# Performance work log

Measured on AMD Instinct MI355X. Metric: run time of the kernel, lower is better.

The kernel has to match this reference:

```python
import jax, jax.numpy as jnp
import numpy as np

CP = 1.0   # polynomial kernel balance (Kerv2d cp)
DP = 2     # polynomial kernel degree (Kerv2d dp)
EPS = 1e-5 # BatchNorm eps


def kerv2d(x, w, stride, padding):
    # polynomial kervolution: (patch . w + cp) ** dp, computed as conv then pointwise
    y = jax.lax.conv_general_dilated(
        x, w,
        window_strides=(stride, stride),
        padding=[(padding, padding), (padding, padding)],
        dimension_numbers=('NCHW', 'OIHW', 'NCHW'))
    return (y + CP) ** DP


def bn(x, g, b, m, v):
    # inference-mode BatchNorm2d with running stats, folded to scale/shift
    inv = g / jnp.sqrt(v + EPS)
    return x * inv[None, :, None, None] + (b - m * inv)[None, :, None, None]


def setup_inputs() -> dict:
    key = jax.random.key(0)
    ks = jax.random.split(key, 4)
    C_in, C_mid = 1024, 256  # bottleneck: 1024 -> 256 -> 256 -> 1024
    d = {
        'x':  jax.random.normal(ks[0], (128, C_in, 14, 14), jnp.float32),
        'w1': jax.random.normal(ks[1], (C_mid, C_in, 1, 1), jnp.float32) * 0.03,
        'w2': jax.random.normal(ks[2], (C_mid, C_mid, 3, 3), jnp.float32) * 0.02,
        'w3': jax.random.normal(ks[3], (C_in, C_mid, 1, 1), jnp.float32) * 0.03,
    }
    for i, c in zip((1, 2, 3), (C_mid, C_mid, C_in)):
        d[f'g{i}'] = jnp.ones((c,), jnp.float32)
        d[f'b{i}'] = jnp.zeros((c,), jnp.float32)
        d[f'm{i}'] = jnp.zeros((c,), jnp.float32)
        d[f'v{i}'] = jnp.ones((c,), jnp.float32)
    return d


def reference(x, w1, w2, w3, g1, b1, m1, v1, g2, b2, m2, v2, g3, b3, m3, v3):
    identity = x
    h = bn(kerv2d(x, w1, 1, 0), g1, b1, m1, v1)   # 1x1 kerv + BN (num_layers>34 branch)
    h = bn(kerv2d(h, w2, 1, 1), g2, b2, m2, v2)   # 3x3 kerv + BN, stride=1
    h = bn(kerv2d(h, w3, 1, 0), g3, b3, m3, v3)   # 1x1 kerv (expansion=4) + BN
    return h + identity                           # residual add (identity_downsample=None)
```

## Files before the change

### kernel.cpp

```cpp
#include <hip/hip_runtime.h>

using f32x4 = __attribute__((ext_vector_type(4))) float;
using s16x8 = __attribute__((ext_vector_type(8))) short;
using s16x4 = __attribute__((ext_vector_type(4))) short;

#define P_PIX 196
#define NPIX_ALL (128 * 196)
#define NROW  208
#define KT    32

static __device__ __forceinline__ short f2bf(float f) {
  union { float f; unsigned u; } a; a.f = f;
  unsigned u = a.u;
  u += 0x7fffu + ((u >> 16) & 1u);
  return (short)(u >> 16);
}

static __device__ __forceinline__ f32x4 mfma16(s16x8 a, s16x8 b, f32x4 c) {
  return __builtin_amdgcn_mfma_f32_16x16x32_bf16(a, b, c, 0, 0, 0);
}

static __device__ __forceinline__ void gload16(const short* g, short* l) {
  __builtin_amdgcn_global_load_lds(
      (const __attribute__((address_space(1))) unsigned int*)(g),
      (__attribute__((address_space(3))) unsigned int*)(l), 16, 0, 0);
}

static __device__ __forceinline__ const s16x8* fragp(const short* buf, int row, int l4) {
  return (const s16x8*)(buf + row * KT + ((l4 ^ ((row >> 1) & 3)) << 3));
}

static __device__ __forceinline__ void stage(const short* __restrict__ src, int srcK,
                                             int k0, short* dst, int rows, int rmax,
                                             int tid, int nthr) {
  for (int t = tid; t < rows * 4; t += nthr) {
    int r = t >> 2, c = t & 3;
    int rr = r < rmax ? r : rmax;
    int cs = c ^ ((r >> 1) & 3);
    gload16(src + (size_t)rr * srcK + k0 + cs * 8, dst + t * 8);
  }
}


__global__ void k_prep(const float* __restrict__ w1, const float* __restrict__ w2,
                       const float* __restrict__ w3,
                       const float* g1, const float* b1, const float* m1, const float* v1,
                       const float* g2, const float* b2, const float* m2, const float* v2,
                       const float* g3, const float* b3, const float* m3, const float* v3,
                       float* bn, short* W1b, short* W2t, short* W3b) {
  int i = blockIdx.x * 256 + threadIdx.x;
  if (i < 65536) {
    f32x4 v = *(const f32x4*)(w1 + i * 4);
    s16x4 o;
    o[0] = f2bf(v[0]); o[1] = f2bf(v[1]); o[2] = f2bf(v[2]); o[3] = f2bf(v[3]);
    *(s16x4*)(W1b + i * 4) = o;
  } else if (i < 131072) {
    int q = i - 65536;
    f32x4 v = *(const f32x4*)(w3 + q * 4);
    s16x4 o;
    o[0] = f2bf(v[0]); o[1] = f2bf(v[1]); o[2] = f2bf(v[2]); o[3] = f2bf(v[3]);
    *(s16x4*)(W3b + q * 4) = o;
  } else if (i < 278528) {
    int q = (i - 131072) * 4;
    s16x4 o;
    #pragma unroll
    for (int k = 0; k < 4; ++k) {
      int idx = q + k;
      int s = idx >> 16, rem = idx & 65535;
      int co = rem >> 8, ci = rem & 255;
      o[k] = f2bf(w2[(co * 256 + ci) * 9 + s]);
    }
    *(s16x4*)(W2t + q) = o;
  } else if (i < 280064) {
    int t = i - 278528;
    if (t < 256) {
      float inv = g1[t] * rsqrtf(v1[t] + 1e-5f);
      bn[t] = inv; bn[256 + t] = b1[t] - m1[t] * inv;
    } else if (t < 512) {
      int c = t - 256;
      float inv = g2[c] * rsqrtf(v2[c] + 1e-5f);
      bn[512 + c] = inv; bn[768 + c] = b2[c] - m2[c] * inv;
    } else {
      int c = t - 512;
      float inv = g3[c] * rsqrtf(v3[c] + 1e-5f);
      bn[1024 + c] = inv; bn[2048 + c] = b3[c] - m3[c] * inv;
    }
  }
}


__global__ __launch_bounds__(256) void k_layer1(
    const float* __restrict__ x, const short* __restrict__ W1b,
    const float* __restrict__ bnbuf, short* __restrict__ H1) {
  __shared__ __align__(16) short lB[2][128 * KT];
  const int tid = threadIdx.x;
  const int vb = (blockIdx.x & 7) * 64 + (blockIdx.x >> 3);
  const int n = vb >> 2, mb = (vb >> 1) & 1, jh = vb & 1;
  const int lane = tid & 63, wave = tid >> 6;
  const int l15 = lane & 15, l4 = lane >> 4;

  if (jh == 1 && tid < 96) {
    int bb = tid / 48, idx = tid % 48;
    s16x8 z = {0,0,0,0,0,0,0,0};
    *(s16x8*)(&lB[bb][100 * KT + idx * 8]) = z;
  }

  const float* xs = x + (size_t)n * 1024 * P_PIX;
  const short* Asrc = W1b + (size_t)(mb * 128) * 1024;

  const int npg = jh ? 25 : 28;
  const int pgbase = jh ? 24 : 0;
  const bool act = tid < npg * 8;
  const int pg = pgbase + (act ? tid % npg : 0);
  const int kg = act ? tid / npg : 0;
  const int lrow0 = pg * 4 - jh * 96;

  f32x4 rX[4], rY[4];
  auto loadx = [&](int kt, f32x4* r) {
    if (!act) return;
    const float* sp = xs + (size_t)(kt * 32 + kg * 4) * P_PIX + pg * 4;
    r[0] = *(const f32x4*)sp;
    r[1] = *(const f32x4*)(sp + P_PIX);
    r[2] = *(const f32x4*)(sp + 2 * P_PIX);
    r[3] = *(const f32x4*)(sp + 3 * P_PIX);
  };
  auto cvtw = [&](const f32x4* r, short* buf) {
    if (!act) return;
    int chunk = kg >> 1, inner = (kg & 1) * 4;
    #pragma unroll
    for (int q = 0; q < 4; ++q) {
      int lr = lrow0 + q;
      s16x4 w;
      w[0] = f2bf(r[0][q]); w[1] = f2bf(r[1][q]);
      w[2] = f2bf(r[2][q]); w[3] = f2bf(r[3][q]);
      *(s16x4*)(buf + lr * KT + ((chunk ^ ((lr >> 1) & 3)) << 3) + inner) = w;
    }
  };

  f32x4 acc[2][7];
  f32x4 zero = {0.f, 0.f, 0.f, 0.f};
  #pragma unroll
  for (int m = 0; m < 2; ++m)
    #pragma unroll
    for (int jj = 0; jj < 7; ++jj) acc[m][jj] = zero;

  loadx(0, rX);
  loadx(1, rY);
  cvtw(rX, lB[0]);
  __syncthreads();

  auto body = [&](int kt, f32x4* rNext, f32x4* rFill) {
    if (kt + 2 < 32) loadx(kt + 2, rFill);
    s16x8 a0 = *(const s16x8*)(Asrc + (size_t)(wave * 32 + l15) * 1024 + kt * 32 + l4 * 8);
    s16x8 a1 = *(const s16x8*)(Asrc + (size_t)(wave * 32 + 16 + l15) * 1024 + kt * 32 + l4 * 8);
    const short* B = lB[kt & 1];
    #pragma unroll
    for (int jj = 0; jj < 7; ++jj) {
      s16x8 bfr = *fragp(B, jj * 16 + l15, l4);
      acc[0][jj] = mfma16(a0, bfr, acc[0][jj]);
      acc[1][jj] = mfma16(a1, bfr, acc[1][jj]);
    }
    if (kt + 1 < 32) cvtw(rNext, lB[(kt + 1) & 1]);
    __syncthreads();
  };

  for (int kt = 0; kt < 32; kt += 2) {
    body(kt, rY, rX);
    body(kt + 1, rX, rY);
  }

  short* Hn = H1 + (size_t)n * P_PIX * 256;
  #pragma unroll
  for (int m = 0; m < 2; ++m) {
    int co = mb * 128 + wave * 32 + m * 16 + l4 * 4;
    f32x4 sc = *(const f32x4*)(bnbuf + co);
    f32x4 sh = *(const f32x4*)(bnbuf + 256 + co);
    #pragma unroll
    for (int jj = 0; jj < 7; ++jj) {
      if (jh && jj == 0) continue;
      int p = (jh * 6 + jj) * 16 + l15;
      if (p < P_PIX) {
        s16x4 o;
        #pragma unroll
        for (int i = 0; i < 4; ++i) {
          float y = acc[m][jj][i] + 1.0f;
          o[i] = f2bf(y * y * sc[i] + sh[i]);
        }
        *(s16x4*)(Hn + p * 256 + co) = o;
      }
    }
  }
}


__global__ __launch_bounds__(512) void k_layer2(
    const short* __restrict__ H1, const short* __restrict__ W2t,
    const float* __restrict__ bnbuf, short* __restrict__ H2) {
  __shared__ __align__(16) short lB[2][NROW * KT];
  const int tid = threadIdx.x;
  const int b = blockIdx.x;
  const int n = b >> 2, mb = (b >> 1) & 1, jh = b & 1;
  const int lane = tid & 63, wave = tid >> 6;
  const int l15 = lane & 15, l4 = lane >> 4;

  if (tid < 8) {
    int bb = tid >> 2, idx = tid & 3;
    s16x8 z = {0,0,0,0,0,0,0,0};
    *(s16x8*)(&lB[bb][196 * KT + idx * 8]) = z;
  }

  int vm[7];
  #pragma unroll
  for (int jj = 0; jj < 7; ++jj) {
    int p = (jh * 6 + jj) * 16 + l15;
    int m = 0;
    if (p < P_PIX) {
      int h = p / 14, w = p % 14;
      m = 2 | 16;
      if (h >= 1)  m |= 1;
      if (h < 13)  m |= 4;
      if (w >= 1)  m |= 8;
      if (w < 13)  m |= 32;
    }
    vm[jj] = m;
  }

  f32x4 acc[7];
  f32x4 zero = {0.f, 0.f, 0.f, 0.f};
  #pragma unroll
  for (int jj = 0; jj < 7; ++jj) acc[jj] = zero;

  const short* Bsrc = H1 + (size_t)n * P_PIX * 256;
  const short* Wbase = W2t + (size_t)(mb * 128 + wave * 16 + l15) * 256 + l4 * 8;

  stage(Bsrc, 256, 0, lB[0], P_PIX, P_PIX - 1, tid, 512);
  __syncthreads();

  for (int kt = 0; kt < 8; ++kt) {
    if (kt < 7)
      stage(Bsrc, 256, (kt + 1) * 32, lB[(kt + 1) & 1], P_PIX, P_PIX - 1, tid, 512);
    const short* B = lB[kt & 1];
    #pragma unroll
    for (int s = 0; s < 9; ++s) {
      const int dy = s / 3, dx = s % 3;
      const int doff = (dy - 1) * 14 + (dx - 1);
      s16x8 a0 = *(const s16x8*)(Wbase + (size_t)(s * 256) * 256 + kt * 32);
      #pragma unroll
      for (int jj = 0; jj < 7; ++jj) {
        int p = (jh * 6 + jj) * 16 + l15;
        bool valid = ((vm[jj] >> dy) & 1) && ((vm[jj] >> (3 + dx)) & 1);
        int row = valid ? (p + doff) : 196;
        s16x8 bfr = *fragp(B, row, l4);
        acc[jj] = mfma16(a0, bfr, acc[jj]);
      }
    }
    __syncthreads();
  }

  short* Hn = H2 + (size_t)n * P_PIX * 256;
  {
    int co = mb * 128 + wave * 16 + l4 * 4;
    f32x4 sc = *(const f32x4*)(bnbuf + 512 + co);
    f32x4 sh = *(const f32x4*)(bnbuf + 768 + co);
    #pragma unroll
    for (int jj = 0; jj < 7; ++jj) {
      if (jh && jj == 0) continue;
      int p = (jh * 6 + jj) * 16 + l15;
      if (p < P_PIX) {
        s16x4 o;
        #pragma unroll
        for (int i = 0; i < 4; ++i) {
          float y = acc[jj][i] + 1.0f;
          o[i] = f2bf(y * y * sc[i] + sh[i]);
        }
        *(s16x4*)(Hn + p * 256 + co) = o;
      }
    }
  }
}


__global__ __launch_bounds__(256) void k_layer3(
    const short* __restrict__ H2, const short* __restrict__ W3b,
    const float* __restrict__ bnbuf, const float* __restrict__ x,
    float* __restrict__ out) {
  __shared__ __align__(16) char smem[27136];
  short* const lB0 = (short*)smem;
  short* const lB1 = lB0 + NROW * KT;
  float* const eb = (float*)smem;

  const int tid = threadIdx.x;
  const int vb = (blockIdx.x & 7) * 256 + (blockIdx.x >> 3);
  const int n = vb >> 4, mb = vb & 15;
  const int lane = tid & 63, wave = tid >> 6;
  const int l15 = lane & 15, l4 = lane >> 4;

  const short* Asrc = W3b + (size_t)(mb * 64) * 256;
  const short* Bsrc = H2 + (size_t)n * P_PIX * 256;

  f32x4 acc[13];
  f32x4 zero = {0.f, 0.f, 0.f, 0.f};
  #pragma unroll
  for (int j = 0; j < 13; ++j) acc[j] = zero;

  stage(Bsrc, 256, 0, lB0, NROW, P_PIX - 1, tid, 256);
  __syncthreads();

  for (int kt = 0; kt < 8; ++kt) {
    s16x8 a = *(const s16x8*)(Asrc + (size_t)(wave * 16 + l15) * 256 + kt * 32 + l4 * 8);
    if (kt < 7)
      stage(Bsrc, 256, (kt + 1) * 32, ((kt + 1) & 1) ? lB1 : lB0, NROW, P_PIX - 1, tid, 256);
    const short* B = (kt & 1) ? lB1 : lB0;
    #pragma unroll
    for (int j = 0; j < 13; ++j) {
      s16x8 bfr = *fragp(B, j * 16 + l15, l4);
      acc[j] = mfma16(a, bfr, acc[j]);
    }
    __syncthreads();
  }

  const int co_r = tid >> 3;
  const int pcb  = tid & 7;
  #pragma unroll
  for (int h = 0; h < 2; ++h) {
    __syncthreads();
    if ((wave >> 1) == h) {
      const int co_l = (wave & 1) * 16 + l4 * 4;
      #pragma unroll
      for (int j = 0; j < 13; ++j) {
        const int p = j * 16 + l15;
        #pragma unroll
        for (int i = 0; i < 4; ++i)
          eb[(co_l + i) * 212 + p] = acc[j][i];
      }
    }
    __syncthreads();
    const int co_g = mb * 64 + h * 32 + co_r;
    const float scv = bnbuf[1024 + co_g];
    const float shv = bnbuf[2048 + co_g];
    const size_t rowbase = ((size_t)(n * 1024 + co_g)) * P_PIX;
    #pragma unroll
    for (int pass = 0; pass < 7; ++pass) {
      const int pc = pcb + pass * 8;
      if (pc < 49) {
        f32x4 v = *(const f32x4*)(eb + co_r * 212 + pc * 4);
        const size_t idx = rowbase + pc * 4;
        f32x4 xv = *(const f32x4*)(x + idx);
        f32x4 o;
        #pragma unroll
        for (int k = 0; k < 4; ++k) {
          float y = v[k] + 1.0f;
          o[k] = y * y * scv + shv + xv[k];
        }
        *(f32x4*)(out + idx) = o;
      }
    }
  }
}


extern "C" void kernel_launch(void* const* d_in, const int* in_sizes, int n_in,
                              void* d_out, int out_size, void* d_ws, size_t ws_size,
                              hipStream_t stream) {
  (void)in_sizes; (void)n_in; (void)out_size; (void)ws_size;
  const float* x  = (const float*)d_in[0];
  const float* w1 = (const float*)d_in[1];
  const float* w2 = (const float*)d_in[2];
  const float* w3 = (const float*)d_in[3];
  const float* g1 = (const float*)d_in[4];
  const float* b1 = (const float*)d_in[5];
  const float* m1 = (const float*)d_in[6];
  const float* v1 = (const float*)d_in[7];
  const float* g2 = (const float*)d_in[8];
  const float* b2 = (const float*)d_in[9];
  const float* m2 = (const float*)d_in[10];
  const float* v2 = (const float*)d_in[11];
  const float* g3 = (const float*)d_in[12];
  const float* b3 = (const float*)d_in[13];
  const float* m3 = (const float*)d_in[14];
  const float* v3 = (const float*)d_in[15];

  char* ws = (char*)d_ws;
  short* W1b   = (short*)(ws + 0);
  short* W2t   = (short*)(ws + 524288);
  short* W3b   = (short*)(ws + 1703936);
  float* bnbuf = (float*)(ws + 2228224);
  short* H1    = (short*)(ws + 2240512);
  short* H2    = (short*)(ws + 15085568);

  k_prep<<<1094, 256, 0, stream>>>(w1, w2, w3,
                                   g1, b1, m1, v1, g2, b2, m2, v2, g3, b3, m3, v3,
                                   bnbuf, W1b, W2t, W3b);
  k_layer1<<<512, 256, 0, stream>>>(x, W1b, bnbuf, H1);
  k_layer2<<<512, 512, 0, stream>>>(H1, W2t, bnbuf, H2);
  k_layer3<<<2048, 256, 0, stream>>>(H2, W3b, bnbuf, x, (float*)d_out);
}
```

Baseline: 155.3 us.

## Stage whole image in LDS for 3x3 layer and cover all output channels per block

The 3x3 kervolution kernel now loads the entire 196x256 bf16 activation tile of an image into LDS once, using an XOR-swizzled layout, instead of double-buffering 32-channel K slices. Each block computes all 256 output channels, with two MFMA accumulator sets per wave, so each B fragment read from LDS feeds two MFMAs. Weight fragments are prefetched one step ahead in registers, and blocks are remapped across XCDs. This removes per-K-step barriers and halves the redundant activation loads, at the cost of about 100KB of LDS per block, a 256-block grid with lower occupancy, and more accumulator registers.

After: 135.7 us (median of 2 runs). 1.14x faster.

```diff
diff --git a/kernel.cpp b/kernel.cpp
--- a/kernel.cpp
+++ b/kernel.cpp
@@ -196,17 +196,22 @@
 __global__ __launch_bounds__(512) void k_layer2(
     const short* __restrict__ H1, const short* __restrict__ W2t,
     const float* __restrict__ bnbuf, short* __restrict__ H2) {
-  __shared__ __align__(16) short lB[2][NROW * KT];
+  __shared__ __align__(16) short lB[197 * 256];
   const int tid = threadIdx.x;
-  const int b = blockIdx.x;
-  const int n = b >> 2, mb = (b >> 1) & 1, jh = b & 1;
+  const int vb = (blockIdx.x & 7) * 32 + (blockIdx.x >> 3);
+  const int n = vb >> 1, jh = vb & 1;
   const int lane = tid & 63, wave = tid >> 6;
   const int l15 = lane & 15, l4 = lane >> 4;
 
-  if (tid < 8) {
-    int bb = tid >> 2, idx = tid & 3;
+  const short* Bsrc = H1 + (size_t)n * P_PIX * 256;
+  for (int t = tid; t < 6272; t += 512) {
+    int row = t >> 5, pc = t & 31;
+    int lc = pc ^ (row & 7);
+    gload16(Bsrc + row * 256 + lc * 8, lB + t * 8);
+  }
+  if (tid < 32) {
     s16x8 z = {0,0,0,0,0,0,0,0};
-    *(s16x8*)(&lB[bb][196 * KT + idx * 8]) = z;
+    *(s16x8*)(&lB[196 * 256 + tid * 8]) = z;
   }
 
   int vm[7];
@@ -225,41 +230,49 @@
     vm[jj] = m;
   }
 
-  f32x4 acc[7];
+  f32x4 acc[2][7];
   f32x4 zero = {0.f, 0.f, 0.f, 0.f};
   #pragma unroll
-  for (int jj = 0; jj < 7; ++jj) acc[jj] = zero;
-
-  const short* Bsrc = H1 + (size_t)n * P_PIX * 256;
-  const short* Wbase = W2t + (size_t)(mb * 128 + wave * 16 + l15) * 256 + l4 * 8;
-
-  stage(Bsrc, 256, 0, lB[0], P_PIX, P_PIX - 1, tid, 512);
+  for (int m = 0; m < 2; ++m)
+    #pragma unroll
+    for (int jj = 0; jj < 7; ++jj) acc[m][jj] = zero;
+
+  auto LA = [&](int kt, int s, int m) -> s16x8 {
+    return *(const s16x8*)(W2t +
+        (size_t)((s * 256 + wave * 32 + m * 16 + l15) * 256) + kt * 32 + l4 * 8);
+  };
+
   __syncthreads();
 
+  s16x8 aC0 = LA(0, 0, 0), aC1 = LA(0, 0, 1);
   for (int kt = 0; kt < 8; ++kt) {
-    if (kt < 7)
-      stage(Bsrc, 256, (kt + 1) * 32, lB[(kt + 1) & 1], P_PIX, P_PIX - 1, tid, 512);
-    const short* B = lB[kt & 1];
+    const int lcb = kt << 2;
     #pragma unroll
     for (int s = 0; s < 9; ++s) {
+      s16x8 aN0 = aC0, aN1 = aC1;
+      const int s1 = (s == 8) ? 0 : s + 1;
+      const int kt1 = (s == 8) ? kt + 1 : kt;
+      if (kt1 < 8) { aN0 = LA(kt1, s1, 0); aN1 = LA(kt1, s1, 1); }
       const int dy = s / 3, dx = s % 3;
       const int doff = (dy - 1) * 14 + (dx - 1);
-      s16x8 a0 = *(const s16x8*)(Wbase + (size_t)(s * 256) * 256 + kt * 32);
       #pragma unroll
       for (int jj = 0; jj < 7; ++jj) {
         int p = (jh * 6 + jj) * 16 + l15;
         bool valid = ((vm[jj] >> dy) & 1) && ((vm[jj] >> (3 + dx)) & 1);
         int row = valid ? (p + doff) : 196;
-        s16x8 bfr = *fragp(B, row, l4);
-        acc[jj] = mfma16(a0, bfr, acc[jj]);
+        int pc = (lcb | l4) ^ (row & 7);
+        s16x8 bfr = *(const s16x8*)(lB + row * 256 + (pc << 3));
+        acc[0][jj] = mfma16(aC0, bfr, acc[0][jj]);
+        acc[1][jj] = mfma16(aC1, bfr, acc[1][jj]);
       }
-    }
-    __syncthreads();
+      aC0 = aN0; aC1 = aN1;
+    }
   }
 
   short* Hn = H2 + (size_t)n * P_PIX * 256;
-  {
-    int co = mb * 128 + wave * 16 + l4 * 4;
+  #pragma unroll
+  for (int m = 0; m < 2; ++m) {
+    int co = wave * 32 + m * 16 + l4 * 4;
     f32x4 sc = *(const f32x4*)(bnbuf + 512 + co);
     f32x4 sh = *(const f32x4*)(bnbuf + 768 + co);
     #pragma unroll
@@ -270,7 +283,7 @@
         s16x4 o;
         #pragma unroll
         for (int i = 0; i < 4; ++i) {
-          float y = acc[jj][i] + 1.0f;
+          float y = acc[m][jj][i] + 1.0f;
           o[i] = f2bf(y * y * sc[i] + sh[i]);
         }
         *(s16x4*)(Hn + p * 256 + co) = o;
@@ -392,6 +405,6 @@
                                    g1, b1, m1, v1, g2, b2, m2, v2, g3, b3, m3, v3,
                                    bnbuf, W1b, W2t, W3b);
   k_layer1<<<512, 256, 0, stream>>>(x, W1b, bnbuf, H1);
-  k_layer2<<<512, 512, 0, stream>>>(H1, W2t, bnbuf, H2);
+  k_layer2<<<256, 512, 0, stream>>>(H1, W2t, bnbuf, H2);
   k_layer3<<<2048, 256, 0, stream>>>(H2, W3b, bnbuf, x, (float*)d_out);
 }
```
